# Kernel optimization log

Hardware: AMD Instinct MI355X
Metric: run time of the kernel (lower is better)

## Reference

```python
import jax, jax.numpy as jnp
import numpy as np
from jax import lax

D = 512        # datapathSize (= slow-net hidden size = embedding size)
H = 20         # nonlinearAfterSlowHiddenSize
V = 32000      # softmaxOutputHeadSize = xEmbeddingsNum
T = 1024       # sequence length (number of sequential fast-weight updates)


def setup_inputs() -> dict:
    key = jax.random.key(0)
    ks = jax.random.split(key, 12)
    inp = {}
    inp["tokens"] = jax.random.randint(ks[0], (T,), 0, V)
    inp["targets"] = jax.random.randint(ks[1], (T,), 0, V)
    # learned parameters
    inp["embed"] = jax.random.normal(ks[2], (V, D), dtype=jnp.float32)
    # fastWeightsInit = rand(D,D) * (1/D)
    inp["fw_init"] = jax.random.uniform(ks[3], (D, D), dtype=jnp.float32) * (1.0 / D)
    inp["eta"] = jnp.array(1.0, dtype=jnp.float32)
    inp["wa"] = jax.random.normal(ks[4], (D, D), dtype=jnp.float32) * 0.05
    inp["wb"] = jax.random.normal(ks[5], (D, D), dtype=jnp.float32) * 0.05
    # nonlinearAfterSlow: Linear(D,H) -> selu -> Linear(H,D); stored as (in,out)
    lim_a = 1.0 / np.sqrt(D)
    inp["mlp_aw"] = jax.random.uniform(ks[6], (D, H), dtype=jnp.float32, minval=-lim_a, maxval=lim_a)
    inp["mlp_ab"] = jax.random.uniform(ks[7], (H,), dtype=jnp.float32, minval=-lim_a, maxval=lim_a)
    lim_b = 1.0 / np.sqrt(H)
    inp["mlp_bw"] = jax.random.uniform(ks[8], (H, D), dtype=jnp.float32, minval=-lim_b, maxval=lim_b)
    inp["mlp_bb"] = jax.random.uniform(ks[9], (D,), dtype=jnp.float32, minval=-lim_b, maxval=lim_b)
    # logit head Linear(D, V)
    inp["head_w"] = jax.random.uniform(ks[10], (D, V), dtype=jnp.float32, minval=-lim_a, maxval=lim_a)
    inp["head_b"] = jax.random.uniform(ks[11], (V,), dtype=jnp.float32, minval=-lim_a, maxval=lim_a)
    return inp


def reference(tokens, targets, embed, fw_init, eta, wa, wb,
              mlp_aw, mlp_ab, mlp_bw, mlp_bb, head_w, head_b):
    xs = embed[tokens]  # [T, D]

    def step(fw, x):
        # SlowNetB.forwardAndUpdate for one token
        z0 = x @ wa                      # [D]
        z1 = x @ wb                      # [D]
        fw_new = jnp.tanh(fw + eta * jnp.outer(z0, z1))  # [D, D]
        y = x @ fw_new                   # [D]
        return fw_new, y

    _, ys = lax.scan(step, fw_init, xs)  # ys: [T, D]

    # NonlinearLayer (batched over T)
    h = jax.nn.selu(ys @ mlp_aw + mlp_ab) @ mlp_bw + mlp_bb  # [T, D]
    mixed = 0.5 * h + 0.5 * xs
    logits = mixed @ head_w + head_b     # [T, V]

    logp = jax.nn.log_softmax(logits, axis=-1)
    loss = -jnp.mean(jnp.take_along_axis(logp, targets[:, None], axis=1))
    return logits, loss
```

## Files before the change

### kernel.cpp

```cpp
#include <hip/hip_runtime.h>

#define D 512
#define H 20
#define V 32000
#define T 1024
#define NT2 500

typedef unsigned int uint;
typedef __attribute__((ext_vector_type(8))) short short8;
typedef __attribute__((ext_vector_type(4))) float floatx4;

__device__ __forceinline__ unsigned short f2bf(float f) {
    unsigned u = __builtin_bit_cast(unsigned, f);
    u += 0x7fffu + ((u >> 16) & 1u);
    return (unsigned short)(u >> 16);
}

template <int CTRL>
__device__ __forceinline__ float dpp_add(float v) {
    int x = __builtin_amdgcn_update_dpp(0, __builtin_bit_cast(int, v), CTRL, 0xf, 0xf, true);
    return v + __builtin_bit_cast(float, x);
}
template <int CTRL>
__device__ __forceinline__ float dpp_max(float v) {
    int x = __builtin_amdgcn_update_dpp(0, __builtin_bit_cast(int, v), CTRL, 0xf, 0xf, true);
    return fmaxf(v, __builtin_bit_cast(float, x));
}
__device__ __forceinline__ float reduce16(float v) {
    v = dpp_add<0xB1>(v);
    v = dpp_add<0x4E>(v);
    v = dpp_add<0x141>(v);
    v = dpp_add<0x140>(v);
    return v;
}
__device__ __forceinline__ float reduce16max(float v) {
    v = dpp_max<0xB1>(v);
    v = dpp_max<0x4E>(v);
    v = dpp_max<0x141>(v);
    v = dpp_max<0x140>(v);
    return v;
}

__global__ __launch_bounds__(256) void gather_kernel(const int* __restrict__ tokens,
                                                     const float* __restrict__ embed,
                                                     float* __restrict__ xs) {
    int idx = blockIdx.x * 256 + threadIdx.x;
    int row = idx >> 7;
    int c   = idx & 127;
    float4 v = ((const float4*)(embed + (long)tokens[row] * D))[c];
    ((float4*)xs)[idx] = v;
}

__global__ __launch_bounds__(256) void zgemm_kernel(const float* __restrict__ xs,
                                                    const float* __restrict__ wa,
                                                    const float* __restrict__ wb,
                                                    float* __restrict__ z0,
                                                    float* __restrict__ z1) {
    __shared__ float Xs[16 * 36];
    __shared__ float Ws[16 * 68];
    const int tid = threadIdx.x;
    const int n0 = blockIdx.x * 64, m0 = blockIdx.y * 32;
    const float* Wm = blockIdx.z ? wb : wa;
    float* Z = blockIdx.z ? z1 : z0;
    const int tx = tid & 15, ty = tid >> 4;
    const int xr = tid >> 3, xk = (tid & 7) * 2;
    const int wr = tid >> 4, wc = (tid & 15) * 4;
    float acc[2][4] = {};
    for (int k0 = 0; k0 < D; k0 += 16) {
        float2 xv = *(const float2*)(xs + (m0 + xr) * D + k0 + xk);
        float4 wv = *(const float4*)(Wm + (k0 + wr) * D + n0 + wc);
        Xs[(xk + 0) * 36 + xr] = xv.x;
        Xs[(xk + 1) * 36 + xr] = xv.y;
        *(float4*)(Ws + wr * 68 + wc) = wv;
        __syncthreads();
#pragma unroll
        for (int k = 0; k < 16; k++) {
            float a0 = Xs[k * 36 + 2 * ty];
            float a1 = Xs[k * 36 + 2 * ty + 1];
            float4 b = *(const float4*)(Ws + k * 68 + tx * 4);
            float bv[4] = {b.x, b.y, b.z, b.w};
#pragma unroll
            for (int c = 0; c < 4; c++) {
                acc[0][c] = __builtin_fmaf(a0, bv[c], acc[0][c]);
                acc[1][c] = __builtin_fmaf(a1, bv[c], acc[1][c]);
            }
        }
        __syncthreads();
    }
    float4 v0 = {acc[0][0], acc[0][1], acc[0][2], acc[0][3]};
    float4 v1 = {acc[1][0], acc[1][1], acc[1][2], acc[1][3]};
    *(float4*)(Z + (m0 + 2 * ty + 0) * D + n0 + tx * 4) = v0;
    *(float4*)(Z + (m0 + 2 * ty + 1) * D + n0 + tx * 4) = v1;
}

#define CC 2.8853900817779268f

#define LOADC(ZA, XA, EC, tbase)                               \
    _Pragma("unroll")                                          \
    for (int c = 0; c < 8; c++) {                              \
        int tr = (tbase + c) * D;                              \
        ZA[c] = z0[tr + i0];                                   \
        XA[c] = xs[tr + i0];                                   \
        EC[c] = z1[tr + j] * ETAC;                             \
    }

#define COMPUTE(ZA, XA, EC, tbase)                             \
    {                                                          \
        float p[8];                                            \
        _Pragma("unroll")                                      \
        for (int c = 0; c < 8; c++) {                          \
            float e0 = __builtin_amdgcn_exp2f(__builtin_fmaf(EC[c], ZA[c], g0)); \
            float r0 = __builtin_amdgcn_rcpf(e0 + 1.0f);       \
            g0 = __builtin_fmaf(-2.0f * CC, r0, CC);           \
            p[c] = XA[c] * g0;                                 \
        }                                                      \
        _Pragma("unroll")                                      \
        for (int c = 0; c < 8; c++) {                          \
            float v = reduce16(p[c]);                          \
            v += __shfl_xor(v, 16, 64);                        \
            v += __shfl_xor(v, 32, 64);                        \
            p[c] = v;                                          \
        }                                                      \
        if (lane == 0) {                                       \
            _Pragma("unroll")                                  \
            for (int c = 0; c < 8; c++) yp[(tbase + c) * D] = p[c]; \
        }                                                      \
    }

__global__ __launch_bounds__(64) void scan_kernel(const float* __restrict__ z0,
                                                  const float* __restrict__ z1,
                                                  const float* __restrict__ xs,
                                                  const float* __restrict__ fw_init,
                                                  const float* __restrict__ eta_p,
                                                  float* __restrict__ ypart) {
    const int lane = threadIdx.x;
    const int bid = blockIdx.x;
    const int j = bid & 511;
    const int q = bid >> 9;
    const int i0 = q * 64 + lane;
    const float eta = *eta_p;
    const float ETAC = eta * CC;
    float g0 = CC * fw_init[(long)i0 * D + j];
    float* yp = ypart + (long)q * T * D + j;

    float zaA[8], xaA[8], ecA[8];
    float zaB[8], xaB[8], ecB[8];
    LOADC(zaA, xaA, ecA, 0);
    for (int t0 = 0; t0 < T; t0 += 16) {
        LOADC(zaB, xaB, ecB, t0 + 8);
        COMPUTE(zaA, xaA, ecA, t0);
        if (t0 + 16 < T) { LOADC(zaA, xaA, ecA, t0 + 16); }
        COMPUTE(zaB, xaB, ecB, t0 + 8);
    }
}

__global__ __launch_bounds__(256) void mlp_fused_kernel(const float* __restrict__ ypart,
                                                        const float* __restrict__ xs,
                                                        const float* __restrict__ Aw,
                                                        const float* __restrict__ Ab,
                                                        const float* __restrict__ Bw,
                                                        const float* __restrict__ Bb,
                                                        unsigned short* __restrict__ mixed) {
    const int t = blockIdx.x, tid = threadIdx.x;
    __shared__ float y_lds[D];
    __shared__ float h_lds[H];
    const float INVC = 0.34657359027997264f;
#pragma unroll
    for (int s = 0; s < 2; s++) {
        int d = s * 256 + tid;
        float v = 0.f;
#pragma unroll
        for (int qq = 0; qq < 8; qq++) v += ypart[((long)qq * T + t) * D + d];
        y_lds[d] = v * INVC;
    }
    __syncthreads();
    const int w = tid >> 6, lane = tid & 63;
    float yv[8];
#pragma unroll
    for (int k = 0; k < 8; k++) yv[k] = y_lds[k * 64 + lane];
#pragma unroll
    for (int u = 0; u < 5; u++) {
        const int jj = w * 5 + u;
        float a = 0.f;
#pragma unroll
        for (int k = 0; k < 8; k++)
            a = __builtin_fmaf(yv[k], Aw[(k * 64 + lane) * H + jj], a);
        a = reduce16(a);
        a += __shfl_xor(a, 16, 64);
        a += __shfl_xor(a, 32, 64);
        if (lane == 0) {
            a += Ab[jj];
            const float sc = 1.0507009873554805f, al = 1.6732632423543772f;
            h_lds[jj] = a > 0.f ? sc * a : sc * al * (__expf(a) - 1.f);
        }
    }
    __syncthreads();
#pragma unroll
    for (int s = 0; s < 2; s++) {
        int d = s * 256 + tid;
        float o = Bb[d];
#pragma unroll
        for (int jj = 0; jj < H; jj++) o = __builtin_fmaf(h_lds[jj], Bw[jj * D + d], o);
        int gi = t * D + d;
        mixed[gi] = f2bf(0.5f * o + 0.5f * xs[gi]);
    }
}

__global__ __launch_bounds__(256) void convert_wt_kernel(const float* __restrict__ head_w,
                                                         unsigned short* __restrict__ wt) {
    __shared__ float tile[64 * 68];
    const int n0 = blockIdx.x * 64, k0 = blockIdx.y * 64;
    const int tid = threadIdx.x;
#pragma unroll
    for (int s = 0; s < 4; s++) {
        int idx4 = s * 256 + tid;
        int r = idx4 >> 4, c4 = idx4 & 15;
        float4 v = *(const float4*)(head_w + (long)(k0 + r) * V + n0 + c4 * 4);
        *(float4*)(tile + r * 68 + c4 * 4) = v;
    }
    __syncthreads();
    const int rr = tid >> 2;
    const int cq = tid & 3;
    uint u[8];
#pragma unroll
    for (int p = 0; p < 8; p++) {
        float a = tile[(cq * 16 + p * 2 + 0) * 68 + rr];
        float b = tile[(cq * 16 + p * 2 + 1) * 68 + rr];
        u[p] = (uint)f2bf(a) | ((uint)f2bf(b) << 16);
    }
    unsigned short* ob = wt + (long)(n0 + rr) * D + k0 + cq * 16;
    uint4 v0 = {u[0], u[1], u[2], u[3]};
    uint4 v1 = {u[4], u[5], u[6], u[7]};
    *(uint4*)ob = v0;
    *((uint4*)ob + 1) = v1;
}

__global__ __launch_bounds__(256) void head_gemm_kernel(const unsigned short* __restrict__ A,
                                                        const unsigned short* __restrict__ Bt,
                                                        const float* __restrict__ bias,
                                                        float* __restrict__ C,
                                                        float* __restrict__ pm,
                                                        float* __restrict__ ps) {
    __shared__ unsigned short As[128 * 64];
    __shared__ unsigned short Bs[128 * 64];
    const int tid = threadIdx.x;
    const int mt = blockIdx.x & 7, nt = blockIdx.x >> 3;
    const int m0 = mt * 128, n0 = nt * 128;
    const int wave = tid >> 6, lane = tid & 63;
    const int wm = wave >> 1, wn = wave & 1;
    const int quad = lane >> 4, l15 = lane & 15;
    floatx4 acc[4][4] = {};
    for (int k0 = 0; k0 < D; k0 += 64) {
#pragma unroll
        for (int s = 0; s < 4; s++) {
            int idx = s * 256 + tid;
            int row = idx >> 3, slot = idx & 7;
            int gch = slot ^ (row & 7);
            const unsigned short* ga = A + (long)(m0 + row) * D + k0 + gch * 8;
            __builtin_amdgcn_global_load_lds(
                (const __attribute__((address_space(1))) unsigned int*)ga,
                (__attribute__((address_space(3))) unsigned int*)(As + idx * 8), 16, 0, 0);
            const unsigned short* gb = Bt + (long)(n0 + row) * D + k0 + gch * 8;
            __builtin_amdgcn_global_load_lds(
                (const __attribute__((address_space(1))) unsigned int*)gb,
                (__attribute__((address_space(3))) unsigned int*)(Bs + idx * 8), 16, 0, 0);
        }
        __syncthreads();
#pragma unroll
        for (int ks = 0; ks < 2; ks++) {
            short8 af[4], bfr[4];
            int q = ks * 4 + quad;
#pragma unroll
            for (int f = 0; f < 4; f++) {
                int ar = wm * 64 + f * 16 + l15;
                af[f] = *(const short8*)(As + ar * 64 + ((q ^ (ar & 7)) * 8));
                int br = wn * 64 + f * 16 + l15;
                bfr[f] = *(const short8*)(Bs + br * 64 + ((q ^ (br & 7)) * 8));
            }
#pragma unroll
            for (int fr = 0; fr < 4; fr++)
#pragma unroll
                for (int fc = 0; fc < 4; fc++)
                    acc[fr][fc] = __builtin_amdgcn_mfma_f32_16x16x32_bf16(af[fr], bfr[fc],
                                                                          acc[fr][fc], 0, 0, 0);
        }
        __syncthreads();
    }
    float bv[4];
#pragma unroll
    for (int fc = 0; fc < 4; fc++) bv[fc] = bias[n0 + wn * 64 + fc * 16 + l15];
#pragma unroll
    for (int fr = 0; fr < 4; fr++) {
        int mr = m0 + wm * 64 + fr * 16 + quad * 4;
#pragma unroll
        for (int r = 0; r < 4; r++) {
            float v[4];
#pragma unroll
            for (int fc = 0; fc < 4; fc++) {
                v[fc] = acc[fr][fc][r] + bv[fc];
                C[(long)(mr + r) * V + n0 + wn * 64 + fc * 16 + l15] = v[fc];
            }
            float mx = fmaxf(fmaxf(v[0], v[1]), fmaxf(v[2], v[3]));
            mx = reduce16max(mx);
            float sv = __expf(v[0] - mx) + __expf(v[1] - mx)
                     + __expf(v[2] - mx) + __expf(v[3] - mx);
            sv = reduce16(sv);
            if (l15 == 0) {
                long row = mr + r;
                pm[row * NT2 + nt * 2 + wn] = mx;
                ps[row * NT2 + nt * 2 + wn] = sv;
            }
        }
    }
}

__device__ __forceinline__ void lse_comb(float& m, float& s, float m2, float s2) {
    float M = fmaxf(m, m2);
    s = s * __expf(m - M) + s2 * __expf(m2 - M);
    m = M;
}

__global__ __launch_bounds__(256) void loss_rows_kernel(const float* __restrict__ pm,
                                                        const float* __restrict__ ps,
                                                        const float* __restrict__ logits,
                                                        const int* __restrict__ targets,
                                                        float* __restrict__ ws_loss) {
    const int t = blockIdx.x, tid = threadIdx.x;
    float m = -INFINITY, s = 0.f;
    for (int i = tid; i < NT2; i += 256)
        lse_comb(m, s, pm[(long)t * NT2 + i], ps[(long)t * NT2 + i]);
#pragma unroll
    for (int msk = 1; msk <= 32; msk <<= 1) {
        float m2 = __shfl_xor(m, msk, 64);
        float s2 = __shfl_xor(s, msk, 64);
        lse_comb(m, s, m2, s2);
    }
    __shared__ float sm[4], ss[4];
    if ((tid & 63) == 0) { sm[tid >> 6] = m; ss[tid >> 6] = s; }
    __syncthreads();
    if (tid == 0) {
        float M = sm[0], S = ss[0];
#pragma unroll
        for (int w = 1; w < 4; w++) lse_comb(M, S, sm[w], ss[w]);
        float lse = M + __logf(S);
        float lt = logits[(long)t * V + targets[t]];
        ws_loss[t] = lse - lt;
    }
}

__global__ __launch_bounds__(256) void loss_final_kernel(const float* __restrict__ ws_loss,
                                                         float* __restrict__ out) {
    const int tid = threadIdx.x;
    float s = 0.f;
    for (int i = tid; i < T; i += 256) s += ws_loss[i];
#pragma unroll
    for (int m = 1; m <= 32; m <<= 1) s += __shfl_xor(s, m, 64);
    __shared__ float red[4];
    if ((tid & 63) == 0) red[tid >> 6] = s;
    __syncthreads();
    if (tid == 0) out[0] = (red[0] + red[1] + red[2] + red[3]) * (1.f / (float)T);
}

extern "C" void kernel_launch(void* const* d_in, const int* in_sizes, int n_in,
                              void* d_out, int out_size, void* d_ws, size_t ws_size,
                              hipStream_t stream) {
    const int*   tokens  = (const int*)d_in[0];
    const int*   targets = (const int*)d_in[1];
    const float* embed   = (const float*)d_in[2];
    const float* fw_init = (const float*)d_in[3];
    const float* eta     = (const float*)d_in[4];
    const float* wa      = (const float*)d_in[5];
    const float* wb      = (const float*)d_in[6];
    const float* mlp_aw  = (const float*)d_in[7];
    const float* mlp_ab  = (const float*)d_in[8];
    const float* mlp_bw  = (const float*)d_in[9];
    const float* mlp_bb  = (const float*)d_in[10];
    const float* head_w  = (const float*)d_in[11];
    const float* head_b  = (const float*)d_in[12];
    float* out = (float*)d_out;

    char* ws = (char*)d_ws;
    float*          xs      = (float*)(ws + 0);
    float*          z0      = (float*)(ws + 2097152);
    float*          z1      = (float*)(ws + 4194304);
    float*          ypart   = (float*)(ws + 6291456);
    unsigned short* wt      = (unsigned short*)(ws + 2097152);
    unsigned short* mixed   = (unsigned short*)(ws + 35651584);
    float*          pm      = (float*)(ws + 36700160);
    float*          psum    = (float*)(ws + 38797312);
    float*          ws_loss = (float*)(ws + 40894464);

    gather_kernel<<<(T * D / 4) / 256, 256, 0, stream>>>(tokens, embed, xs);
    zgemm_kernel<<<dim3(D / 64, T / 32, 2), 256, 0, stream>>>(xs, wa, wb, z0, z1);
    scan_kernel<<<4096, 64, 0, stream>>>(z0, z1, xs, fw_init, eta, ypart);
    mlp_fused_kernel<<<T, 256, 0, stream>>>(ypart, xs, mlp_aw, mlp_ab, mlp_bw, mlp_bb, mixed);
    convert_wt_kernel<<<dim3(V / 64, D / 64), 256, 0, stream>>>(head_w, wt);
    head_gemm_kernel<<<(T / 128) * (V / 128), 256, 0, stream>>>(mixed, wt, head_b, out, pm, psum);
    loss_rows_kernel<<<T, 256, 0, stream>>>(pm, psum, out, targets, ws_loss);
    loss_final_kernel<<<1, 256, 0, stream>>>(ws_loss, out + (long)T * V);
}
```

Baseline: 542.5 us.

## Rework scan to two rows per lane, XCD-aware head tiling, atomic loss

The scan kernel now has each lane own two fast-weight rows via float2 loads. That halves the block count and the number of partial-sum slices, and it uses a four-stage load pipeline with scheduling barriers and nontemporal stores. The eta*C scale is folded into the z0 GEMM epilogue. The head GEMM block index is remapped so that neighbouring N-tiles land on the same XCD, which adds padding blocks that exit early. The final loss reduction kernel is replaced by an atomicAdd in loss_rows, with the accumulator zeroed in the gather kernel. This trades float-summation determinism for one fewer launch.

Result: no change. 549.8 us (+1.3%).

```diff
diff --git a/kernel.cpp b/kernel.cpp
--- a/kernel.cpp
+++ b/kernel.cpp
@@ -9,6 +9,9 @@
 typedef unsigned int uint;
 typedef __attribute__((ext_vector_type(8))) short short8;
 typedef __attribute__((ext_vector_type(4))) float floatx4;
+
+#define CC 2.8853900817779268f
+#define M2C -5.7707801635558537f
 
 __device__ __forceinline__ unsigned short f2bf(float f) {
     unsigned u = __builtin_bit_cast(unsigned, f);
@@ -43,8 +46,10 @@
 
 __global__ __launch_bounds__(256) void gather_kernel(const int* __restrict__ tokens,
                                                      const float* __restrict__ embed,
-                                                     float* __restrict__ xs) {
+                                                     float* __restrict__ xs,
+                                                     float* __restrict__ loss_acc) {
     int idx = blockIdx.x * 256 + threadIdx.x;
+    if (idx == 0) *loss_acc = 0.f;
     int row = idx >> 7;
     int c   = idx & 127;
     float4 v = ((const float4*)(embed + (long)tokens[row] * D))[c];
@@ -54,6 +59,7 @@
 __global__ __launch_bounds__(256) void zgemm_kernel(const float* __restrict__ xs,
                                                     const float* __restrict__ wa,
                                                     const float* __restrict__ wb,
+                                                    const float* __restrict__ eta_p,
                                                     float* __restrict__ z0,
                                                     float* __restrict__ z1) {
     __shared__ float Xs[16 * 36];
@@ -62,6 +68,7 @@
     const int n0 = blockIdx.x * 64, m0 = blockIdx.y * 32;
     const float* Wm = blockIdx.z ? wb : wa;
     float* Z = blockIdx.z ? z1 : z0;
+    const float sc = blockIdx.z ? 1.0f : (*eta_p) * CC;
     const int tx = tid & 15, ty = tid >> 4;
     const int xr = tid >> 3, xk = (tid & 7) * 2;
     const int wr = tid >> 4, wc = (tid & 15) * 4;
@@ -87,70 +94,80 @@
         }
         __syncthreads();
     }
-    float4 v0 = {acc[0][0], acc[0][1], acc[0][2], acc[0][3]};
-    float4 v1 = {acc[1][0], acc[1][1], acc[1][2], acc[1][3]};
+    float4 v0 = {sc * acc[0][0], sc * acc[0][1], sc * acc[0][2], sc * acc[0][3]};
+    float4 v1 = {sc * acc[1][0], sc * acc[1][1], sc * acc[1][2], sc * acc[1][3]};
     *(float4*)(Z + (m0 + 2 * ty + 0) * D + n0 + tx * 4) = v0;
     *(float4*)(Z + (m0 + 2 * ty + 1) * D + n0 + tx * 4) = v1;
 }
 
-#define CC 2.8853900817779268f
-
-#define LOADC(ZA, XA, EC, tbase)                               \
-    _Pragma("unroll")                                          \
-    for (int c = 0; c < 8; c++) {                              \
-        int tr = (tbase + c) * D;                              \
-        ZA[c] = z0[tr + i0];                                   \
-        XA[c] = xs[tr + i0];                                   \
-        EC[c] = z1[tr + j] * ETAC;                             \
-    }
-
-#define COMPUTE(ZA, XA, EC, tbase)                             \
-    {                                                          \
-        float p[8];                                            \
-        _Pragma("unroll")                                      \
-        for (int c = 0; c < 8; c++) {                          \
-            float e0 = __builtin_amdgcn_exp2f(__builtin_fmaf(EC[c], ZA[c], g0)); \
-            float r0 = __builtin_amdgcn_rcpf(e0 + 1.0f);       \
-            g0 = __builtin_fmaf(-2.0f * CC, r0, CC);           \
-            p[c] = XA[c] * g0;                                 \
-        }                                                      \
-        _Pragma("unroll")                                      \
-        for (int c = 0; c < 8; c++) {                          \
-            float v = reduce16(p[c]);                          \
-            v += __shfl_xor(v, 16, 64);                        \
-            v += __shfl_xor(v, 32, 64);                        \
-            p[c] = v;                                          \
-        }                                                      \
-        if (lane == 0) {                                       \
-            _Pragma("unroll")                                  \
-            for (int c = 0; c < 8; c++) yp[(tbase + c) * D] = p[c]; \
-        }                                                      \
+#define LOADC(B, cb)                                                          \
+    {                                                                         \
+        _Pragma("unroll")                                                     \
+        for (int c = 0; c < 8; c++) {                                         \
+            const int tr = ((cb) * 8 + c) * D;                                \
+            za##B[c] = *(const float2*)(z0 + tr + i0);                        \
+            xa##B[c] = *(const float2*)(xs + tr + i0);                        \
+            ez##B[c] = z1[tr + j];                                            \
+        }                                                                     \
+        __builtin_amdgcn_sched_barrier(0);                                    \
+    }
+
+#define COMPUTE(B, cb)                                                        \
+    {                                                                         \
+        float p[8];                                                           \
+        _Pragma("unroll")                                                     \
+        for (int c = 0; c < 8; c++) {                                         \
+            float e = ez##B[c];                                               \
+            float a0 = __builtin_amdgcn_exp2f(__builtin_fmaf(e, za##B[c].x, g0)); \
+            float a1 = __builtin_amdgcn_exp2f(__builtin_fmaf(e, za##B[c].y, g1)); \
+            float r0 = __builtin_amdgcn_rcpf(a0 + 1.0f);                      \
+            float r1 = __builtin_amdgcn_rcpf(a1 + 1.0f);                      \
+            g0 = __builtin_fmaf(M2C, r0, CC);                                 \
+            g1 = __builtin_fmaf(M2C, r1, CC);                                 \
+            p[c] = xa##B[c].x * g0 + xa##B[c].y * g1;                         \
+        }                                                                     \
+        _Pragma("unroll")                                                     \
+        for (int c = 0; c < 8; c++) {                                         \
+            float v = reduce16(p[c]);                                         \
+            v += __shfl_xor(v, 16, 64);                                       \
+            v += __shfl_xor(v, 32, 64);                                       \
+            p[c] = v;                                                         \
+        }                                                                     \
+        if (lane == 0) {                                                      \
+            _Pragma("unroll")                                                 \
+            for (int c = 0; c < 8; c++)                                       \
+                __builtin_nontemporal_store(p[c], yp + ((cb) * 8 + c) * D);   \
+        }                                                                     \
+        __builtin_amdgcn_sched_barrier(0);                                    \
     }
 
 __global__ __launch_bounds__(64) void scan_kernel(const float* __restrict__ z0,
                                                   const float* __restrict__ z1,
                                                   const float* __restrict__ xs,
                                                   const float* __restrict__ fw_init,
-                                                  const float* __restrict__ eta_p,
                                                   float* __restrict__ ypart) {
     const int lane = threadIdx.x;
     const int bid = blockIdx.x;
     const int j = bid & 511;
     const int q = bid >> 9;
-    const int i0 = q * 64 + lane;
-    const float eta = *eta_p;
-    const float ETAC = eta * CC;
+    const int i0 = q * 128 + 2 * lane;
     float g0 = CC * fw_init[(long)i0 * D + j];
+    float g1 = CC * fw_init[(long)(i0 + 1) * D + j];
     float* yp = ypart + (long)q * T * D + j;
 
-    float zaA[8], xaA[8], ecA[8];
-    float zaB[8], xaB[8], ecB[8];
-    LOADC(zaA, xaA, ecA, 0);
-    for (int t0 = 0; t0 < T; t0 += 16) {
-        LOADC(zaB, xaB, ecB, t0 + 8);
-        COMPUTE(zaA, xaA, ecA, t0);
-        if (t0 + 16 < T) { LOADC(zaA, xaA, ecA, t0 + 16); }
-        COMPUTE(zaB, xaB, ecB, t0 + 8);
+    float2 za0[8], xa0[8], za1[8], xa1[8], za2[8], xa2[8], za3[8], xa3[8];
+    float  ez0[8], ez1[8], ez2[8], ez3[8];
+
+    LOADC(0, 0); LOADC(1, 1); LOADC(2, 2);
+    for (int i = 0; i < 128; i += 4) {
+        LOADC(3, i + 3);
+        COMPUTE(0, i);
+        LOADC(0, i + 4);
+        COMPUTE(1, i + 1);
+        LOADC(1, i + 5);
+        COMPUTE(2, i + 2);
+        LOADC(2, i + 6);
+        COMPUTE(3, i + 3);
     }
 }
 
@@ -170,7 +187,8 @@
         int d = s * 256 + tid;
         float v = 0.f;
 #pragma unroll
-        for (int qq = 0; qq < 8; qq++) v += ypart[((long)qq * T + t) * D + d];
+        for (int qq = 0; qq < 4; qq++)
+            v += __builtin_nontemporal_load(ypart + ((long)qq * T + t) * D + d);
         y_lds[d] = v * INVC;
     }
     __syncthreads();
@@ -244,7 +262,11 @@
     __shared__ unsigned short As[128 * 64];
     __shared__ unsigned short Bs[128 * 64];
     const int tid = threadIdx.x;
-    const int mt = blockIdx.x & 7, nt = blockIdx.x >> 3;
+    const int bid = blockIdx.x;
+    const int xcd = bid & 7;
+    const int mt = (bid >> 3) & 7;
+    const int nt = (bid >> 6) * 8 + xcd;
+    if (nt >= V / 128) return;
     const int m0 = mt * 128, n0 = nt * 128;
     const int wave = tid >> 6, lane = tid & 63;
     const int wm = wave >> 1, wn = wave & 1;
@@ -324,7 +346,7 @@
                                                         const float* __restrict__ ps,
                                                         const float* __restrict__ logits,
                                                         const int* __restrict__ targets,
-                                                        float* __restrict__ ws_loss) {
+                                                        float* __restrict__ loss_acc) {
     const int t = blockIdx.x, tid = threadIdx.x;
     float m = -INFINITY, s = 0.f;
     for (int i = tid; i < NT2; i += 256)
@@ -344,21 +366,8 @@
         for (int w = 1; w < 4; w++) lse_comb(M, S, sm[w], ss[w]);
         float lse = M + __logf(S);
         float lt = logits[(long)t * V + targets[t]];
-        ws_loss[t] = lse - lt;
-    }
-}
-
-__global__ __launch_bounds__(256) void loss_final_kernel(const float* __restrict__ ws_loss,
-                                                         float* __restrict__ out) {
-    const int tid = threadIdx.x;
-    float s = 0.f;
-    for (int i = tid; i < T; i += 256) s += ws_loss[i];
-#pragma unroll
-    for (int m = 1; m <= 32; m <<= 1) s += __shfl_xor(s, m, 64);
-    __shared__ float red[4];
-    if ((tid & 63) == 0) red[tid >> 6] = s;
-    __syncthreads();
-    if (tid == 0) out[0] = (red[0] + red[1] + red[2] + red[3]) * (1.f / (float)T);
+        atomicAdd(loss_acc, (lse - lt) * (1.0f / (float)T));
+    }
 }
 
 extern "C" void kernel_launch(void* const* d_in, const int* in_sizes, int n_in,
@@ -378,6 +387,7 @@
     const float* head_w  = (const float*)d_in[11];
     const float* head_b  = (const float*)d_in[12];
     float* out = (float*)d_out;
+    float* loss_acc = out + (long)T * V;
 
     char* ws = (char*)d_ws;
     float*          xs      = (float*)(ws + 0);
@@ -388,14 +398,12 @@
     unsigned short* mixed   = (unsigned short*)(ws + 35651584);
     float*          pm      = (float*)(ws + 36700160);
     float*          psum    = (float*)(ws + 38797312);
-    float*          ws_loss = (float*)(ws + 40894464);
-
-    gather_kernel<<<(T * D / 4) / 256, 256, 0, stream>>>(tokens, embed, xs);
-    zgemm_kernel<<<dim3(D / 64, T / 32, 2), 256, 0, stream>>>(xs, wa, wb, z0, z1);
-    scan_kernel<<<4096, 64, 0, stream>>>(z0, z1, xs, fw_init, eta, ypart);
+
+    gather_kernel<<<(T * D / 4) / 256, 256, 0, stream>>>(tokens, embed, xs, loss_acc);
+    zgemm_kernel<<<dim3(D / 64, T / 32, 2), 256, 0, stream>>>(xs, wa, wb, eta, z0, z1);
+    scan_kernel<<<2048, 64, 0, stream>>>(z0, z1, xs, fw_init, ypart);
     mlp_fused_kernel<<<T, 256, 0, stream>>>(ypart, xs, mlp_aw, mlp_ab, mlp_bw, mlp_bb, mixed);
     convert_wt_kernel<<<dim3(V / 64, D / 64), 256, 0, stream>>>(head_w, wt);
-    head_gemm_kernel<<<(T / 128) * (V / 128), 256, 0, stream>>>(mixed, wt, head_b, out, pm, psum);
-    loss_rows_kernel<<<T, 256, 0, stream>>>(pm, psum, out, targets, ws_loss);
-    loss_final_kernel<<<1, 256, 0, stream>>>(ws_loss, out + (long)T * V);
-}
+    head_gemm_kernel<<<2048, 256, 0, stream>>>(mixed, wt, head_b, out, pm, psum);
+    loss_rows_kernel<<<T, 256, 0, stream>>>(pm, psum, out, targets, loss_acc);
+}
```
